# Optimization experiments

Measured on AMD Instinct MI355X. Metric: run time of the kernel, lower is better.

Reference implementation:

```python
import jax, jax.numpy as jnp
import numpy as np

K = 512      # fixed candidate budget per pyramid level (batched stand-in for mask.nonzero)
THR = 0.5    # candidate threshold from `p > 0.5`
CUBE = 4     # z-2 : z+2 -> 4-voxel cube per axis


def _conv3d(x, w, b, stride):
    y = jax.lax.conv_general_dilated(
        x, w, (stride, stride, stride), 'SAME',
        dimension_numbers=('NCDHW', 'OIDHW', 'NCDHW'))
    return y + b[None, :, None, None, None]


def _up2(x):
    return jnp.repeat(jnp.repeat(jnp.repeat(x, 2, axis=2), 2, axis=3), 2, axis=4)


def _extract(p):
    # p: [1, C, D, H, W] -> (cubes [K, C, 4, 4, 4], valid [K])
    p0 = p[0]
    C, D, H, W = p0.shape
    score = p0.max(axis=0)                       # [D, H, W] peak over channels
    vals, idx = jax.lax.top_k(score.reshape(-1), K)
    valid = (vals > THR).astype(p0.dtype)        # mask out sub-threshold slots
    z = idx // (H * W)
    rem = idx % (H * W)
    y = rem // W
    x = rem % W
    zs = jnp.clip(z - 2, 0, D - CUBE)
    ys = jnp.clip(y - 2, 0, H - CUBE)
    xs = jnp.clip(x - 2, 0, W - CUBE)

    def cube(zi, yi, xi):
        return jax.lax.dynamic_slice(p0, (0, zi, yi, xi), (C, CUBE, CUBE, CUBE))

    return jax.vmap(cube)(zs, ys, xs), valid


def _lhi(cubes):
    # local intensity descriptor: per-channel mean + std over the cube
    m = cubes.mean(axis=(2, 3, 4))
    s = jnp.sqrt(cubes.var(axis=(2, 3, 4)) + 1e-6)
    return jnp.concatenate([m, s], axis=-1)      # [K, 2C]


def _forward(x, c1w, c1b, c2w, c2b, c3w, c3b,
             l1w, l1b, l2w, l2b, l3w, l3b, w1, b1, w2, b2):
    # Encoder3D: 3 strided conv blocks
    f1 = jax.nn.relu(_conv3d(x, c1w, c1b, 2))    # [1,16,48,96,96]
    f2 = jax.nn.relu(_conv3d(f1, c2w, c2b, 2))   # [1,32,24,48,48]
    f3 = jax.nn.relu(_conv3d(f2, c3w, c3b, 2))   # [1,64,12,24,24]
    # FeaturePyramid3D: laterals + top-down adds
    p3 = _conv3d(f3, l3w, l3b, 1)
    p2 = _conv3d(f2, l2w, l2b, 1) + _up2(p3)
    p1 = _conv3d(f1, l1w, l1b, 1) + _up2(p2)
    outs = []
    for p in (p1, p2, p3):
        cubes, valid = _extract(p)
        lhi = _lhi(cubes)                        # [K, 64]
        h = jax.nn.relu(lhi @ w1 + b1)
        o = (h @ w2 + b2) * valid[:, None]       # zero out invalid candidate slots
        outs.append(o)
    return jnp.concatenate(outs, axis=0)         # [3K, 2]


def setup_inputs() -> dict:
    key = jax.random.key(0)
    ks = jax.random.split(key, 10)

    def w(k, shape, scale):
        return jax.random.normal(k, shape, jnp.float32) * scale

    return {
        'x':   jax.random.normal(ks[0], (1, 1, 96, 192, 192), jnp.float32),
        'c1w': w(ks[1], (16, 1, 3, 3, 3), 0.3),  'c1b': jnp.zeros((16,), jnp.float32),
        'c2w': w(ks[2], (32, 16, 3, 3, 3), 0.1), 'c2b': jnp.zeros((32,), jnp.float32),
        'c3w': w(ks[3], (64, 32, 3, 3, 3), 0.08), 'c3b': jnp.zeros((64,), jnp.float32),
        'l1w': w(ks[4], (32, 16, 1, 1, 1), 0.3), 'l1b': jnp.zeros((32,), jnp.float32),
        'l2w': w(ks[5], (32, 32, 1, 1, 1), 0.3), 'l2b': jnp.zeros((32,), jnp.float32),
        'l3w': w(ks[6], (32, 64, 1, 1, 1), 0.3), 'l3b': jnp.zeros((32,), jnp.float32),
        'w1':  w(ks[7], (64, 128), 0.2),         'b1':  jnp.zeros((128,), jnp.float32),
        'w2':  w(ks[8], (128, 2), 0.2),          'b2':  jnp.zeros((2,), jnp.float32),
    }


def reference(x, c1w, c1b, c2w, c2b, c3w, c3b,
              l1w, l1b, l2w, l2b, l3w, l3b, w1, b1, w2, b2):
    return _forward(x, c1w, c1b, c2w, c2b, c3w, c3b,
                    l1w, l1b, l2w, l2b, l3w, l3b, w1, b1, w2, b2)
```

## Files before the change

### kernel.cpp

```cpp
#include <hip/hip_runtime.h>
#include <hip/hip_bf16.h>
#include <cstdint>
#include <cstddef>

#define N1 442368
#define N2 55296
#define N3 6912

#define PZ1 9409
#define PN1 461041
#define PV1 461041
#define PZ2 2401
#define PN2 60025
#define PV2 60025

#define KCAND 512
#define CAP   4096

__device__ __forceinline__ unsigned long long f2key64(double f) {
  unsigned long long b = (unsigned long long)__double_as_longlong(f);
  return (b & 0x8000000000000000ULL) ? ~b : (b | 0x8000000000000000ULL);
}
__device__ __forceinline__ unsigned f2key32(float f) {
  unsigned b = __float_as_uint(f);
  return (b & 0x80000000u) ? ~b : (b | 0x80000000u);
}

__global__ __launch_bounds__(256) void conv1_k(const float* __restrict__ x, const float* __restrict__ w,
                                               const float* __restrict__ b, double* __restrict__ f1) {
  __shared__ __align__(16) double wsD[27 * 16];
  for (int i = threadIdx.x; i < 27 * 16; i += 256) {
    int t = i >> 4, c = i & 15;
    wsD[i] = (double)w[c * 27 + t];
  }
  __syncthreads();
  int v = blockIdx.x * 256 + threadIdx.x;
  if (v >= PV1) return;
  int z = v / PZ1; int r = v % PZ1; int y = r / 97; int xo = r % 97;
  if (z >= 48 || y >= 96 || xo >= 96) {
#pragma unroll
    for (int c = 0; c < 16; c++) f1[(size_t)c * PN1 + v] = 0.0;
    return;
  }
  float val[27];
#pragma unroll
  for (int dz = 0; dz < 3; dz++)
#pragma unroll
    for (int dy = 0; dy < 3; dy++)
#pragma unroll
      for (int dx = 0; dx < 3; dx++) {
        int zi = 2 * z + dz, yi = 2 * y + dy, xi = 2 * xo + dx;
        bool ok = (zi < 96) & (yi < 192) & (xi < 192);
        int zc = min(zi, 95), yc = min(yi, 191), xc = min(xi, 191);
        float t = x[(zc * 192 + yc) * 192 + xc];
        val[(dz * 3 + dy) * 3 + dx] = ok ? t : 0.0f;
      }
  double acc[16];
#pragma unroll
  for (int c = 0; c < 16; c++) acc[c] = (double)b[c];
#pragma unroll
  for (int t = 0; t < 27; t++) {
    double vv = (double)val[t];
#pragma unroll
    for (int c = 0; c < 16; c++) acc[c] = fma(vv, wsD[t * 16 + c], acc[c]);
  }
#pragma unroll
  for (int c = 0; c < 16; c++) f1[(size_t)c * PN1 + v] = fmax(acc[c], 0.0);
}

__global__ __launch_bounds__(256) void conv2_k(const double* __restrict__ f1, const float* __restrict__ w,
                                               const float* __restrict__ b, double* __restrict__ f2) {
  __shared__ __align__(16) double wsD[16 * 27 * 16];
  int g = blockIdx.y;
  for (int i = threadIdx.x; i < 16 * 27 * 16; i += 256) {
    int ci = i / 432, rem = i % 432, t = rem >> 4, c = rem & 15;
    wsD[i] = (double)w[((size_t)(g * 16 + c) * 16 + ci) * 27 + t];
  }
  __syncthreads();
  int v = blockIdx.x * 256 + threadIdx.x;
  if (v >= PV2) return;
  int z = v / PZ2; int r = v % PZ2; int y = r / 49; int xo = r % 49;
  if (z >= 24 || y >= 48 || xo >= 48) {
#pragma unroll
    for (int c = 0; c < 16; c++) f2[(size_t)(g * 16 + c) * PN2 + v] = 0.0;
    return;
  }
  double acc[16];
#pragma unroll
  for (int c = 0; c < 16; c++) acc[c] = (double)b[g * 16 + c];
  const double* base = f1 + (size_t)(2 * z) * PZ1 + (2 * y) * 97 + 2 * xo;
  for (int ci = 0; ci < 16; ci++) {
    const double* fp = base + (size_t)ci * PN1;
    double vals[27];
#pragma unroll
    for (int dz = 0; dz < 3; dz++)
#pragma unroll
      for (int dy = 0; dy < 3; dy++)
#pragma unroll
        for (int dx = 0; dx < 3; dx++)
          vals[(dz * 3 + dy) * 3 + dx] = fp[dz * PZ1 + dy * 97 + dx];
#pragma unroll
    for (int t = 0; t < 27; t++) {
      double vv = vals[t];
      const double* wp = &wsD[(ci * 27 + t) * 16];
#pragma unroll
      for (int c = 0; c < 16; c++) acc[c] = fma(vv, wp[c], acc[c]);
    }
  }
#pragma unroll
  for (int c = 0; c < 16; c++) f2[(size_t)(g * 16 + c) * PN2 + v] = fmax(acc[c], 0.0);
}

__global__ __launch_bounds__(256) void conv3_k(const double* __restrict__ f2, const float* __restrict__ w,
                                               const float* __restrict__ b, double* __restrict__ f3) {
  __shared__ __align__(16) double wsD[32 * 27 * 4];
  int g = blockIdx.y;
  for (int i = threadIdx.x; i < 32 * 27 * 4; i += 256) {
    int ci = i / 108, rem = i % 108, t = rem >> 2, c = rem & 3;
    wsD[i] = (double)w[((size_t)(g * 4 + c) * 32 + ci) * 27 + t];
  }
  __syncthreads();
  int v = blockIdx.x * 256 + threadIdx.x;
  if (v >= N3) return;
  int z = v / 576; int r = v % 576; int y = r / 24; int xo = r % 24;
  double acc[4];
#pragma unroll
  for (int c = 0; c < 4; c++) acc[c] = (double)b[g * 4 + c];
  const double* base = f2 + (size_t)(2 * z) * PZ2 + (2 * y) * 49 + 2 * xo;
  for (int ci = 0; ci < 32; ci++) {
    const double* fp = base + (size_t)ci * PN2;
    double vals[27];
#pragma unroll
    for (int dz = 0; dz < 3; dz++)
#pragma unroll
      for (int dy = 0; dy < 3; dy++)
#pragma unroll
        for (int dx = 0; dx < 3; dx++)
          vals[(dz * 3 + dy) * 3 + dx] = fp[dz * PZ2 + dy * 49 + dx];
#pragma unroll
    for (int t = 0; t < 27; t++) {
      double vv = vals[t];
      const double* wp = &wsD[(ci * 27 + t) * 4];
#pragma unroll
      for (int c = 0; c < 4; c++) acc[c] = fma(vv, wp[c], acc[c]);
    }
  }
#pragma unroll
  for (int c = 0; c < 4; c++) f3[(size_t)(g * 4 + c) * N3 + v] = fmax(acc[c], 0.0);
}

__global__ __launch_bounds__(256) void p3_k(const double* __restrict__ f3, const float* __restrict__ w,
                                            const float* __restrict__ b, double* __restrict__ p3d,
                                            float* __restrict__ p3f, double* __restrict__ s3) {
  __shared__ __align__(16) double wsD[64 * 32];
  for (int i = threadIdx.x; i < 64 * 32; i += 256) {
    int ci = i >> 5, c = i & 31;
    wsD[i] = (double)w[c * 64 + ci];
  }
  __syncthreads();
  int v = blockIdx.x * 256 + threadIdx.x;
  if (v >= N3) return;
  double acc[32];
#pragma unroll
  for (int c = 0; c < 32; c++) acc[c] = (double)b[c];
  for (int ci = 0; ci < 64; ci++) {
    double vv = f3[(size_t)ci * N3 + v];
    const double* wp = &wsD[ci * 32];
#pragma unroll
    for (int c = 0; c < 32; c++) acc[c] = fma(vv, wp[c], acc[c]);
  }
  double m = -1e300;
#pragma unroll
  for (int c = 0; c < 32; c++) {
    p3d[(size_t)c * N3 + v] = acc[c];
    p3f[(size_t)c * N3 + v] = (float)acc[c];
    m = fmax(m, acc[c]);
  }
  s3[v] = m;
}

__global__ __launch_bounds__(256) void p2_k(const double* __restrict__ f2, const float* __restrict__ w,
                                            const float* __restrict__ b, const double* __restrict__ p3d,
                                            double* __restrict__ p2d, float* __restrict__ p2f, double* __restrict__ s2) {
  __shared__ __align__(16) double wsD[32 * 32];
  for (int i = threadIdx.x; i < 32 * 32; i += 256) {
    int ci = i >> 5, c = i & 31;
    wsD[i] = (double)w[c * 32 + ci];
  }
  __syncthreads();
  int v = blockIdx.x * 256 + threadIdx.x;
  if (v >= N2) return;
  int z = v / (48 * 48); int r = v % (48 * 48); int y = r / 48; int xo = r % 48;
  int pidx = z * PZ2 + y * 49 + xo;
  int up = ((z >> 1) * 24 + (y >> 1)) * 24 + (xo >> 1);
  double acc[32];
#pragma unroll
  for (int c = 0; c < 32; c++) acc[c] = (double)b[c];
  for (int ci = 0; ci < 32; ci++) {
    double vv = f2[(size_t)ci * PN2 + pidx];
    const double* wp = &wsD[ci * 32];
#pragma unroll
    for (int c = 0; c < 32; c++) acc[c] = fma(vv, wp[c], acc[c]);
  }
  double m = -1e300;
#pragma unroll
  for (int c = 0; c < 32; c++) {
    double o = acc[c] + p3d[(size_t)c * N3 + up];
    p2d[(size_t)c * N2 + v] = o;
    p2f[(size_t)c * N2 + v] = (float)o;
    m = fmax(m, o);
  }
  s2[v] = m;
}

__global__ __launch_bounds__(256) void p1_k(const double* __restrict__ f1, const float* __restrict__ w,
                                            const float* __restrict__ b, const double* __restrict__ p2d,
                                            double* __restrict__ s1) {
  __shared__ __align__(16) double wsD[16 * 32];
  for (int i = threadIdx.x; i < 16 * 32; i += 256) {
    int ci = i >> 5, c = i & 31;
    wsD[i] = (double)w[c * 16 + ci];
  }
  __syncthreads();
  int v = blockIdx.x * 256 + threadIdx.x;
  if (v >= N1) return;
  int z = v / (96 * 96); int r = v % (96 * 96); int y = r / 96; int xo = r % 96;
  int pidx = z * PZ1 + y * 97 + xo;
  int up = ((z >> 1) * 48 + (y >> 1)) * 48 + (xo >> 1);
  double acc[32];
#pragma unroll
  for (int c = 0; c < 32; c++) acc[c] = (double)b[c];
  for (int ci = 0; ci < 16; ci++) {
    double vv = f1[(size_t)ci * PN1 + pidx];
    const double* wp = &wsD[ci * 32];
#pragma unroll
    for (int c = 0; c < 32; c++) acc[c] = fma(vv, wp[c], acc[c]);
  }
  double m = -1e300;
#pragma unroll
  for (int c = 0; c < 32; c++) m = fmax(m, acc[c] + p2d[(size_t)c * N2 + up]);
  s1[v] = m;
}

__global__ void hist1_k(const double* __restrict__ s1, const double* __restrict__ s2,
                        const double* __restrict__ s3, unsigned* __restrict__ hist) {
  int L = blockIdx.y;
  const double* s = L == 0 ? s1 : (L == 1 ? s2 : s3);
  int n = L == 0 ? N1 : (L == 1 ? N2 : N3);
  unsigned* hg = hist + L * 256;
  __shared__ unsigned h[256];
  h[threadIdx.x] = 0;
  __syncthreads();
  for (int i = blockIdx.x * 256 + threadIdx.x; i < n; i += gridDim.x * 256)
    atomicAdd(&h[f2key32((float)s[i]) >> 24], 1u);
  __syncthreads();
  unsigned v = h[threadIdx.x];
  if (v) atomicAdd(&hg[threadIdx.x], v);
}

__global__ void pick1_k(const unsigned* __restrict__ hist, unsigned* __restrict__ meta) {
  int L = threadIdx.x;
  if (L >= 3) return;
  const unsigned* hg = hist + L * 256;
  unsigned run = 0; int b = 0;
  for (int i = 255; i >= 0; i--) {
    unsigned c = hg[i];
    if (run + c >= (unsigned)KCAND) { b = i; break; }
    run += c;
  }
  meta[L * 4 + 0] = (unsigned)b;
  meta[L * 4 + 1] = run;
}

__global__ void hist2_k(const double* __restrict__ s1, const double* __restrict__ s2,
                        const double* __restrict__ s3, const unsigned* __restrict__ meta,
                        unsigned* __restrict__ hist2) {
  int L = blockIdx.y;
  const double* s = L == 0 ? s1 : (L == 1 ? s2 : s3);
  int n = L == 0 ? N1 : (L == 1 ? N2 : N3);
  unsigned b1 = meta[L * 4 + 0];
  unsigned* hg = hist2 + L * 256;
  __shared__ unsigned h[256];
  h[threadIdx.x] = 0;
  __syncthreads();
  for (int i = blockIdx.x * 256 + threadIdx.x; i < n; i += gridDim.x * 256) {
    unsigned k = f2key32((float)s[i]);
    if ((k >> 24) == b1) atomicAdd(&h[(k >> 16) & 255u], 1u);
  }
  __syncthreads();
  unsigned v = h[threadIdx.x];
  if (v) atomicAdd(&hg[threadIdx.x], v);
}

__global__ void pick2_k(const unsigned* __restrict__ hist2, unsigned* __restrict__ meta) {
  int L = threadIdx.x;
  if (L >= 3) return;
  const unsigned* hg = hist2 + L * 256;
  unsigned b1 = meta[L * 4 + 0];
  unsigned run = meta[L * 4 + 1];
  unsigned b2 = 0;
  for (int i = 255; i >= 0; i--) {
    run += hg[i];
    if (run >= (unsigned)KCAND) { b2 = (unsigned)i; break; }
  }
  meta[L * 4 + 2] = (b1 << 24) | (b2 << 16);
}

__global__ void compact_k(const double* __restrict__ s1, const double* __restrict__ s2,
                          const double* __restrict__ s3, const unsigned* __restrict__ meta,
                          unsigned long long* __restrict__ ck, unsigned* __restrict__ cidx,
                          unsigned* __restrict__ cnt) {
  int L = blockIdx.y;
  const double* s = L == 0 ? s1 : (L == 1 ? s2 : s3);
  int n = L == 0 ? N1 : (L == 1 ? N2 : N3);
  unsigned T = meta[L * 4 + 2];
  for (int i = blockIdx.x * 256 + threadIdx.x; i < n; i += gridDim.x * 256) {
    double v = s[i];
    if (f2key32((float)v) >= T) {
      unsigned pos = atomicAdd(&cnt[L], 1u);
      if (pos < (unsigned)CAP) {
        ck[(size_t)L * CAP + pos] = f2key64(v);
        cidx[(size_t)L * CAP + pos] = (unsigned)i;
      }
    }
  }
}

__global__ void sort_k(const unsigned long long* __restrict__ ckA, const unsigned* __restrict__ cidxA,
                       const unsigned* __restrict__ cnt, uint2* __restrict__ topkA) {
  __shared__ unsigned long long k_[CAP];
  __shared__ unsigned x_[CAP];
  int L = blockIdx.x;
  const unsigned long long* ck = ckA + (size_t)L * CAP;
  const unsigned* cidx = cidxA + (size_t)L * CAP;
  uint2* topk = topkA + (size_t)L * KCAND;
  int t = threadIdx.x;
  unsigned m = cnt[L]; if (m > (unsigned)CAP) m = CAP;
  int sz = 512; while (sz < (int)m) sz <<= 1;
  for (int i = t; i < sz; i += 1024) {
    if (i < (int)m) { k_[i] = ck[i]; x_[i] = cidx[i]; }
    else            { k_[i] = 0ULL;  x_[i] = 0xFFFFFFFFu; }
  }
  __syncthreads();
  for (int kk = 2; kk <= sz; kk <<= 1) {
    for (int j = kk >> 1; j > 0; j >>= 1) {
      for (int i = t; i < sz; i += 1024) {
        int l = i ^ j;
        if (l > i) {
          unsigned long long ka = k_[i], kb = k_[l];
          unsigned ia = x_[i], ib = x_[l];
          bool b_first = (kb > ka) || (kb == ka && ib < ia);
          bool up = (i & kk) == 0;
          if (up == b_first) { k_[i] = kb; x_[i] = ib; k_[l] = ka; x_[l] = ia; }
        }
      }
      __syncthreads();
    }
  }
  if (t < KCAND) {
    unsigned long long key = k_[t];
    unsigned long long bb = (key >> 63) ? (key & 0x7FFFFFFFFFFFFFFFULL) : ~key;
    double sc = __longlong_as_double((long long)bb);
    topk[t] = make_uint2(x_[t], sc > 0.5 ? 1u : 0u);
  }
}

__global__ __launch_bounds__(64) void mlp_k(const uint2* __restrict__ topkA,
                                            const double* __restrict__ f1d, const double* __restrict__ p2d,
                                            const float* __restrict__ p2f, const float* __restrict__ p3f,
                                            const float* __restrict__ l1w, const float* __restrict__ l1b,
                                            const float* __restrict__ w1, const float* __restrict__ b1,
                                            const float* __restrict__ w2, const float* __restrict__ b2,
                                            float* __restrict__ out) {
  __shared__ double lhi[64];
  __shared__ double f1c[16 * 64];
  __shared__ double wsD[16 * 32];
  int L = blockIdx.y;
  int s = blockIdx.x;
  int D = 48 >> L, H = 96 >> L, W = 96 >> L;
  uint2 e = topkA[(size_t)L * KCAND + s];
  unsigned idx = e.x;
  double valid = e.y ? 1.0 : 0.0;
  int HW = H * W;
  int z = (int)(idx / (unsigned)HW);
  int r = (int)(idx % (unsigned)HW);
  int y = r / W; int x = r % W;
  int zs = min(max(z - 2, 0), D - 4);
  int ys = min(max(y - 2, 0), H - 4);
  int xs = min(max(x - 2, 0), W - 4);
  int t = threadIdx.x;
  int c = t & 31, h = t >> 5;
  double sum = 0.0, ss = 0.0;
  if (L == 0) {
    for (int i = t; i < 512; i += 64) wsD[i] = (double)l1w[(i & 31) * 16 + (i >> 5)];
    for (int i = t; i < 1024; i += 64) {
      int ci = i >> 6, v = i & 63;
      int dz = v >> 4, dy = (v >> 2) & 3, dx = v & 3;
      f1c[i] = f1d[(size_t)ci * PN1 + (zs + dz) * PZ1 + (ys + dy) * 97 + (xs + dx)];
    }
    __syncthreads();
    double bc = (double)l1b[c];
    for (int i = 0; i < 32; i++) {
      int vv = h * 32 + i;
      int dz = vv >> 4, dy = (vv >> 2) & 3, dx = vv & 3;
      int up = (((zs + dz) >> 1) * 48 + ((ys + dy) >> 1)) * 48 + ((xs + dx) >> 1);
      double val = bc + p2d[(size_t)c * N2 + up];
#pragma unroll
      for (int ci = 0; ci < 16; ci++)
        val = fma(f1c[ci * 64 + vv], wsD[ci * 32 + c], val);
      sum += val; ss = fma(val, val, ss);
    }
  } else {
    const float* p = (L == 1) ? p2f : p3f;
    const float* pc = p + (size_t)c * D * HW;
    for (int i = 0; i < 32; i++) {
      int vv = h * 32 + i;
      int dz = vv >> 4, dy = (vv >> 2) & 3, dx = vv & 3;
      double val = (double)pc[(zs + dz) * HW + (ys + dy) * W + (xs + dx)];
      sum += val; ss = fma(val, val, ss);
    }
  }
  sum += __shfl_xor(sum, 32);
  ss  += __shfl_xor(ss, 32);
  if (h == 0) {
    double mean = sum * (1.0 / 64.0);
    double var = ss * (1.0 / 64.0) - mean * mean;
    lhi[c] = mean;
    lhi[32 + c] = sqrt(var + 1e-6);
  }
  __syncthreads();
  double h0 = (double)b1[t], h1 = (double)b1[t + 64];
  for (int i = 0; i < 64; i++) {
    double li = lhi[i];
    h0 = fma(li, (double)w1[i * 128 + t], h0);
    h1 = fma(li, (double)w1[i * 128 + t + 64], h1);
  }
  h0 = fmax(h0, 0.0); h1 = fmax(h1, 0.0);
  double o0 = h0 * (double)w2[t * 2 + 0] + h1 * (double)w2[(t + 64) * 2 + 0];
  double o1 = h0 * (double)w2[t * 2 + 1] + h1 * (double)w2[(t + 64) * 2 + 1];
  for (int o = 1; o < 64; o <<= 1) { o0 += __shfl_xor(o0, o); o1 += __shfl_xor(o1, o); }
  if (t == 0) {
    out[((size_t)L * KCAND + s) * 2 + 0] = (float)((o0 + (double)b2[0]) * valid);
    out[((size_t)L * KCAND + s) * 2 + 1] = (float)((o1 + (double)b2[1]) * valid);
  }
}

extern "C" void kernel_launch(void* const* d_in, const int* in_sizes, int n_in,
                              void* d_out, int out_size, void* d_ws, size_t ws_size,
                              hipStream_t stream) {
  const float* x   = (const float*)d_in[0];
  const float* c1w = (const float*)d_in[1];  const float* c1b = (const float*)d_in[2];
  const float* c2w = (const float*)d_in[3];  const float* c2b = (const float*)d_in[4];
  const float* c3w = (const float*)d_in[5];  const float* c3b = (const float*)d_in[6];
  const float* l1w = (const float*)d_in[7];  const float* l1b = (const float*)d_in[8];
  const float* l2w = (const float*)d_in[9];  const float* l2b = (const float*)d_in[10];
  const float* l3w = (const float*)d_in[11]; const float* l3b = (const float*)d_in[12];
  const float* w1  = (const float*)d_in[13]; const float* b1  = (const float*)d_in[14];
  const float* w2  = (const float*)d_in[15]; const float* b2  = (const float*)d_in[16];
  float* out = (float*)d_out;

  char* ws = (char*)d_ws;
  size_t off = 0;
  auto take = [&](size_t bytes) { size_t o = off; off = (off + bytes + 255) & ~(size_t)255; return o; };
  double* f1d = (double*)(ws + take((size_t)16 * PN1 * 8));
  double* f2d = (double*)(ws + take((size_t)32 * PN2 * 8));
  double* f3d = (double*)(ws + take((size_t)64 * N3 * 8));
  double* p2d = (double*)(ws + take((size_t)32 * N2 * 8));
  float*  p2f = (float*) (ws + take((size_t)32 * N2 * 4));
  double* p3d = (double*)(ws + take((size_t)32 * N3 * 8));
  float*  p3f = (float*) (ws + take((size_t)32 * N3 * 4));
  double* s1 = (double*)(ws + take((size_t)N1 * 8));
  double* s2 = (double*)(ws + take((size_t)N2 * 8));
  double* s3 = (double*)(ws + take((size_t)N3 * 8));
  size_t zOff = take((3 * 256 + 3 * 256 + 3) * 4);
  unsigned* hist1 = (unsigned*)(ws + zOff);
  unsigned* hist2 = hist1 + 3 * 256;
  unsigned* cnt   = hist2 + 3 * 256;
  unsigned* meta  = (unsigned*)(ws + take(12 * 4));
  unsigned long long* candKey = (unsigned long long*)(ws + take((size_t)3 * CAP * 8));
  unsigned* candIdx = (unsigned*)(ws + take((size_t)3 * CAP * 4));
  uint2* topk = (uint2*)(ws + take((size_t)3 * KCAND * 8));

  hipMemsetAsync(ws + zOff, 0, (3 * 256 + 3 * 256 + 3) * 4, stream);

  conv1_k<<<(PV1 + 255) / 256, 256, 0, stream>>>(x, c1w, c1b, f1d);
  conv2_k<<<dim3((PV2 + 255) / 256, 2), 256, 0, stream>>>(f1d, c2w, c2b, f2d);
  conv3_k<<<dim3(N3 / 256, 16), 256, 0, stream>>>(f2d, c3w, c3b, f3d);
  p3_k<<<N3 / 256, 256, 0, stream>>>(f3d, l3w, l3b, p3d, p3f, s3);
  p2_k<<<N2 / 256, 256, 0, stream>>>(f2d, l2w, l2b, p3d, p2d, p2f, s2);
  p1_k<<<N1 / 256, 256, 0, stream>>>(f1d, l1w, l1b, p2d, s1);

  hist1_k<<<dim3(64, 3), 256, 0, stream>>>(s1, s2, s3, hist1);
  pick1_k<<<1, 64, 0, stream>>>(hist1, meta);
  hist2_k<<<dim3(64, 3), 256, 0, stream>>>(s1, s2, s3, meta, hist2);
  pick2_k<<<1, 64, 0, stream>>>(hist2, meta);
  compact_k<<<dim3(112, 3), 256, 0, stream>>>(s1, s2, s3, meta, candKey, candIdx, cnt);
  sort_k<<<3, 1024, 0, stream>>>(candKey, candIdx, cnt, topk);
  mlp_k<<<dim3(KCAND, 3), 64, 0, stream>>>(topk, f1d, p2d, p2f, p3f, l1w, l1b,
                                           w1, b1, w2, b2, out);
}
```

Measured before the change: 445.5 us.

## De-interleave even/odd x columns in f1/f2, widen conv3 channels, fold pick kernels

Stores f1 and f2 with even x columns first and odd columns after (MAP1/MAP2). The stride-2 convolutions in conv2 and conv3 then read contiguous rows across adjacent threads instead of stride-2 gathers, and every consumer of f1/f2 (p1, p2, mlp) is updated to the new indexing. conv3 now computes 8 output channels per thread with half the grid, so each input value loaded is reused across more outputs. The pick1/pick2 threshold kernels are removed; each block of hist2 and compact rescans the histograms itself, which saves launches at the cost of redundant serial loops in every block.

```diff
diff --git a/kernel.cpp b/kernel.cpp
--- a/kernel.cpp
+++ b/kernel.cpp
@@ -14,6 +14,9 @@
 #define PN2 60025
 #define PV2 60025
 
+#define MAP1(x) (((x) & 1) ? 49 + ((x) >> 1) : ((x) >> 1))
+#define MAP2(x) (((x) & 1) ? 25 + ((x) >> 1) : ((x) >> 1))
+
 #define KCAND 512
 #define CAP   4096
 
@@ -37,9 +40,10 @@
   int v = blockIdx.x * 256 + threadIdx.x;
   if (v >= PV1) return;
   int z = v / PZ1; int r = v % PZ1; int y = r / 97; int xo = r % 97;
+  int ov = z * PZ1 + y * 97 + MAP1(xo);
   if (z >= 48 || y >= 96 || xo >= 96) {
 #pragma unroll
-    for (int c = 0; c < 16; c++) f1[(size_t)c * PN1 + v] = 0.0;
+    for (int c = 0; c < 16; c++) f1[(size_t)c * PN1 + ov] = 0.0;
     return;
   }
   float val[27];
@@ -65,7 +69,7 @@
     for (int c = 0; c < 16; c++) acc[c] = fma(vv, wsD[t * 16 + c], acc[c]);
   }
 #pragma unroll
-  for (int c = 0; c < 16; c++) f1[(size_t)c * PN1 + v] = fmax(acc[c], 0.0);
+  for (int c = 0; c < 16; c++) f1[(size_t)c * PN1 + ov] = fmax(acc[c], 0.0);
 }
 
 __global__ __launch_bounds__(256) void conv2_k(const double* __restrict__ f1, const float* __restrict__ w,
@@ -80,25 +84,29 @@
   int v = blockIdx.x * 256 + threadIdx.x;
   if (v >= PV2) return;
   int z = v / PZ2; int r = v % PZ2; int y = r / 49; int xo = r % 49;
+  int ov = z * PZ2 + y * 49 + MAP2(xo);
   if (z >= 24 || y >= 48 || xo >= 48) {
 #pragma unroll
-    for (int c = 0; c < 16; c++) f2[(size_t)(g * 16 + c) * PN2 + v] = 0.0;
+    for (int c = 0; c < 16; c++) f2[(size_t)(g * 16 + c) * PN2 + ov] = 0.0;
     return;
   }
   double acc[16];
 #pragma unroll
   for (int c = 0; c < 16; c++) acc[c] = (double)b[g * 16 + c];
-  const double* base = f1 + (size_t)(2 * z) * PZ1 + (2 * y) * 97 + 2 * xo;
+  const double* base = f1 + (size_t)(2 * z) * PZ1 + (2 * y) * 97;
   for (int ci = 0; ci < 16; ci++) {
     const double* fp = base + (size_t)ci * PN1;
     double vals[27];
 #pragma unroll
     for (int dz = 0; dz < 3; dz++)
 #pragma unroll
-      for (int dy = 0; dy < 3; dy++)
-#pragma unroll
-        for (int dx = 0; dx < 3; dx++)
-          vals[(dz * 3 + dy) * 3 + dx] = fp[dz * PZ1 + dy * 97 + dx];
+      for (int dy = 0; dy < 3; dy++) {
+        const double* row = fp + dz * PZ1 + dy * 97;
+        int o = (dz * 3 + dy) * 3;
+        vals[o + 0] = row[xo];
+        vals[o + 1] = row[49 + xo];
+        vals[o + 2] = row[xo + 1];
+      }
 #pragma unroll
     for (int t = 0; t < 27; t++) {
       double vv = vals[t];
@@ -108,45 +116,48 @@
     }
   }
 #pragma unroll
-  for (int c = 0; c < 16; c++) f2[(size_t)(g * 16 + c) * PN2 + v] = fmax(acc[c], 0.0);
+  for (int c = 0; c < 16; c++) f2[(size_t)(g * 16 + c) * PN2 + ov] = fmax(acc[c], 0.0);
 }
 
 __global__ __launch_bounds__(256) void conv3_k(const double* __restrict__ f2, const float* __restrict__ w,
                                                const float* __restrict__ b, double* __restrict__ f3) {
-  __shared__ __align__(16) double wsD[32 * 27 * 4];
+  __shared__ __align__(16) double wsD[32 * 27 * 8];
   int g = blockIdx.y;
-  for (int i = threadIdx.x; i < 32 * 27 * 4; i += 256) {
-    int ci = i / 108, rem = i % 108, t = rem >> 2, c = rem & 3;
-    wsD[i] = (double)w[((size_t)(g * 4 + c) * 32 + ci) * 27 + t];
+  for (int i = threadIdx.x; i < 32 * 27 * 8; i += 256) {
+    int ci = i / 216, rem = i % 216, t = rem >> 3, c = rem & 7;
+    wsD[i] = (double)w[((size_t)(g * 8 + c) * 32 + ci) * 27 + t];
   }
   __syncthreads();
   int v = blockIdx.x * 256 + threadIdx.x;
   if (v >= N3) return;
   int z = v / 576; int r = v % 576; int y = r / 24; int xo = r % 24;
-  double acc[4];
-#pragma unroll
-  for (int c = 0; c < 4; c++) acc[c] = (double)b[g * 4 + c];
-  const double* base = f2 + (size_t)(2 * z) * PZ2 + (2 * y) * 49 + 2 * xo;
+  double acc[8];
+#pragma unroll
+  for (int c = 0; c < 8; c++) acc[c] = (double)b[g * 8 + c];
+  const double* base = f2 + (size_t)(2 * z) * PZ2 + (2 * y) * 49;
   for (int ci = 0; ci < 32; ci++) {
     const double* fp = base + (size_t)ci * PN2;
     double vals[27];
 #pragma unroll
     for (int dz = 0; dz < 3; dz++)
 #pragma unroll
-      for (int dy = 0; dy < 3; dy++)
-#pragma unroll
-        for (int dx = 0; dx < 3; dx++)
-          vals[(dz * 3 + dy) * 3 + dx] = fp[dz * PZ2 + dy * 49 + dx];
+      for (int dy = 0; dy < 3; dy++) {
+        const double* row = fp + dz * PZ2 + dy * 49;
+        int o = (dz * 3 + dy) * 3;
+        vals[o + 0] = row[xo];
+        vals[o + 1] = row[25 + xo];
+        vals[o + 2] = row[xo + 1];
+      }
 #pragma unroll
     for (int t = 0; t < 27; t++) {
       double vv = vals[t];
-      const double* wp = &wsD[(ci * 27 + t) * 4];
-#pragma unroll
-      for (int c = 0; c < 4; c++) acc[c] = fma(vv, wp[c], acc[c]);
-    }
-  }
-#pragma unroll
-  for (int c = 0; c < 4; c++) f3[(size_t)(g * 4 + c) * N3 + v] = fmax(acc[c], 0.0);
+      const double* wp = &wsD[(ci * 27 + t) * 8];
+#pragma unroll
+      for (int c = 0; c < 8; c++) acc[c] = fma(vv, wp[c], acc[c]);
+    }
+  }
+#pragma unroll
+  for (int c = 0; c < 8; c++) f3[(size_t)(g * 8 + c) * N3 + v] = fmax(acc[c], 0.0);
 }
 
 __global__ __launch_bounds__(256) void p3_k(const double* __restrict__ f3, const float* __restrict__ w,
@@ -191,7 +202,7 @@
   int v = blockIdx.x * 256 + threadIdx.x;
   if (v >= N2) return;
   int z = v / (48 * 48); int r = v % (48 * 48); int y = r / 48; int xo = r % 48;
-  int pidx = z * PZ2 + y * 49 + xo;
+  int pidx = z * PZ2 + y * 49 + MAP2(xo);
   int up = ((z >> 1) * 24 + (y >> 1)) * 24 + (xo >> 1);
   double acc[32];
 #pragma unroll
@@ -225,7 +236,7 @@
   int v = blockIdx.x * 256 + threadIdx.x;
   if (v >= N1) return;
   int z = v / (96 * 96); int r = v % (96 * 96); int y = r / 96; int xo = r % 96;
-  int pidx = z * PZ1 + y * 97 + xo;
+  int pidx = z * PZ1 + y * 97 + MAP1(xo);
   int up = ((z >> 1) * 48 + (y >> 1)) * 48 + (xo >> 1);
   double acc[32];
 #pragma unroll
@@ -258,27 +269,19 @@
   if (v) atomicAdd(&hg[threadIdx.x], v);
 }
 
-__global__ void pick1_k(const unsigned* __restrict__ hist, unsigned* __restrict__ meta) {
-  int L = threadIdx.x;
-  if (L >= 3) return;
-  const unsigned* hg = hist + L * 256;
-  unsigned run = 0; int b = 0;
-  for (int i = 255; i >= 0; i--) {
-    unsigned c = hg[i];
-    if (run + c >= (unsigned)KCAND) { b = i; break; }
-    run += c;
-  }
-  meta[L * 4 + 0] = (unsigned)b;
-  meta[L * 4 + 1] = run;
-}
-
 __global__ void hist2_k(const double* __restrict__ s1, const double* __restrict__ s2,
-                        const double* __restrict__ s3, const unsigned* __restrict__ meta,
+                        const double* __restrict__ s3, const unsigned* __restrict__ hist1,
                         unsigned* __restrict__ hist2) {
   int L = blockIdx.y;
   const double* s = L == 0 ? s1 : (L == 1 ? s2 : s3);
   int n = L == 0 ? N1 : (L == 1 ? N2 : N3);
-  unsigned b1 = meta[L * 4 + 0];
+  const unsigned* h1 = hist1 + L * 256;
+  unsigned run = 0; unsigned b1 = 0;
+  for (int i = 255; i >= 0; i--) {
+    unsigned c = h1[i];
+    if (run + c >= (unsigned)KCAND) { b1 = (unsigned)i; break; }
+    run += c;
+  }
   unsigned* hg = hist2 + L * 256;
   __shared__ unsigned h[256];
   h[threadIdx.x] = 0;
@@ -292,28 +295,28 @@
   if (v) atomicAdd(&hg[threadIdx.x], v);
 }
 
-__global__ void pick2_k(const unsigned* __restrict__ hist2, unsigned* __restrict__ meta) {
-  int L = threadIdx.x;
-  if (L >= 3) return;
-  const unsigned* hg = hist2 + L * 256;
-  unsigned b1 = meta[L * 4 + 0];
-  unsigned run = meta[L * 4 + 1];
-  unsigned b2 = 0;
-  for (int i = 255; i >= 0; i--) {
-    run += hg[i];
-    if (run >= (unsigned)KCAND) { b2 = (unsigned)i; break; }
-  }
-  meta[L * 4 + 2] = (b1 << 24) | (b2 << 16);
-}
-
 __global__ void compact_k(const double* __restrict__ s1, const double* __restrict__ s2,
-                          const double* __restrict__ s3, const unsigned* __restrict__ meta,
+                          const double* __restrict__ s3, const unsigned* __restrict__ hist1,
+                          const unsigned* __restrict__ hist2,
                           unsigned long long* __restrict__ ck, unsigned* __restrict__ cidx,
                           unsigned* __restrict__ cnt) {
   int L = blockIdx.y;
   const double* s = L == 0 ? s1 : (L == 1 ? s2 : s3);
   int n = L == 0 ? N1 : (L == 1 ? N2 : N3);
-  unsigned T = meta[L * 4 + 2];
+  const unsigned* h1 = hist1 + L * 256;
+  const unsigned* h2 = hist2 + L * 256;
+  unsigned run = 0; unsigned b1 = 0;
+  for (int i = 255; i >= 0; i--) {
+    unsigned c = h1[i];
+    if (run + c >= (unsigned)KCAND) { b1 = (unsigned)i; break; }
+    run += c;
+  }
+  unsigned b2 = 0;
+  for (int i = 255; i >= 0; i--) {
+    run += h2[i];
+    if (run >= (unsigned)KCAND) { b2 = (unsigned)i; break; }
+  }
+  unsigned T = (b1 << 24) | (b2 << 16);
   for (int i = blockIdx.x * 256 + threadIdx.x; i < n; i += gridDim.x * 256) {
     double v = s[i];
     if (f2key32((float)v) >= T) {
@@ -396,7 +399,7 @@
     for (int i = t; i < 1024; i += 64) {
       int ci = i >> 6, v = i & 63;
       int dz = v >> 4, dy = (v >> 2) & 3, dx = v & 3;
-      f1c[i] = f1d[(size_t)ci * PN1 + (zs + dz) * PZ1 + (ys + dy) * 97 + (xs + dx)];
+      f1c[i] = f1d[(size_t)ci * PN1 + (zs + dz) * PZ1 + (ys + dy) * 97 + MAP1(xs + dx)];
     }
     __syncthreads();
     double bc = (double)l1b[c];
@@ -476,7 +479,6 @@
   unsigned* hist1 = (unsigned*)(ws + zOff);
   unsigned* hist2 = hist1 + 3 * 256;
   unsigned* cnt   = hist2 + 3 * 256;
-  unsigned* meta  = (unsigned*)(ws + take(12 * 4));
   unsigned long long* candKey = (unsigned long long*)(ws + take((size_t)3 * CAP * 8));
   unsigned* candIdx = (unsigned*)(ws + take((size_t)3 * CAP * 4));
   uint2* topk = (uint2*)(ws + take((size_t)3 * KCAND * 8));
@@ -485,16 +487,14 @@
 
   conv1_k<<<(PV1 + 255) / 256, 256, 0, stream>>>(x, c1w, c1b, f1d);
   conv2_k<<<dim3((PV2 + 255) / 256, 2), 256, 0, stream>>>(f1d, c2w, c2b, f2d);
-  conv3_k<<<dim3(N3 / 256, 16), 256, 0, stream>>>(f2d, c3w, c3b, f3d);
+  conv3_k<<<dim3(N3 / 256, 8), 256, 0, stream>>>(f2d, c3w, c3b, f3d);
   p3_k<<<N3 / 256, 256, 0, stream>>>(f3d, l3w, l3b, p3d, p3f, s3);
   p2_k<<<N2 / 256, 256, 0, stream>>>(f2d, l2w, l2b, p3d, p2d, p2f, s2);
   p1_k<<<N1 / 256, 256, 0, stream>>>(f1d, l1w, l1b, p2d, s1);
 
   hist1_k<<<dim3(64, 3), 256, 0, stream>>>(s1, s2, s3, hist1);
-  pick1_k<<<1, 64, 0, stream>>>(hist1, meta);
-  hist2_k<<<dim3(64, 3), 256, 0, stream>>>(s1, s2, s3, meta, hist2);
-  pick2_k<<<1, 64, 0, stream>>>(hist2, meta);
-  compact_k<<<dim3(112, 3), 256, 0, stream>>>(s1, s2, s3, meta, candKey, candIdx, cnt);
+  hist2_k<<<dim3(64, 3), 256, 0, stream>>>(s1, s2, s3, hist1, hist2);
+  compact_k<<<dim3(112, 3), 256, 0, stream>>>(s1, s2, s3, hist1, hist2, candKey, candIdx, cnt);
   sort_k<<<3, 1024, 0, stream>>>(candKey, candIdx, cnt, topk);
   mlp_k<<<dim3(KCAND, 3), 64, 0, stream>>>(topk, f1d, p2d, p2f, p3f, l1w, l1b,
                                            w1, b1, w2, b2, out);
```

Result: no change. 453.5 us (+1.8%).
